# Kernel tuning notes

Measured on AMD Instinct MI355X. Metric: run time of the kernel, lower is better.

## Reference

```python
import jax, jax.numpy as jnp
import numpy as np

N_NODES = 50000
N_EDGES = 800000
D_IN = 256
D_OUT = 256


def setup_inputs() -> dict:
    key = jax.random.key(0)
    ks = jax.random.split(key, 8)
    x = jax.random.normal(ks[0], (N_NODES, D_IN), dtype=jnp.float32)
    edge_index = jax.random.randint(ks[1], (2, N_EDGES), 0, N_NODES, dtype=jnp.int64)
    W_src = jax.random.normal(ks[2], (D_IN, D_OUT), dtype=jnp.float32) * 0.05
    b_src = jax.random.normal(ks[3], (D_OUT,), dtype=jnp.float32) * 0.05
    W_dst = jax.random.normal(ks[4], (D_IN, D_OUT), dtype=jnp.float32) * 0.05
    b_dst = jax.random.normal(ks[5], (D_OUT,), dtype=jnp.float32) * 0.05
    W_self = jax.random.normal(ks[6], (D_IN, D_OUT), dtype=jnp.float32) * 0.05
    b_self = jax.random.normal(ks[7], (D_OUT,), dtype=jnp.float32) * 0.05
    return {"x": x, "edge_index": edge_index, "W_src": W_src, "b_src": b_src,
            "W_dst": W_dst, "b_dst": b_dst, "W_self": W_self, "b_self": b_self}


def reference(x, edge_index, W_src, b_src, W_dst, b_dst, W_self, b_self):
    # LEConv: messages = src_linear(x[row]) - dst_linear(x[col]);
    # scatter-add messages into destination nodes (col); add self_linear(x).
    # Linear commutes with row-gather, so project once on [N, d] then gather.
    row, col = edge_index[0], edge_index[1]
    src = x @ W_src + b_src            # [N, D_OUT]
    dst = x @ W_dst + b_dst            # [N, D_OUT]
    messages = src[row] - dst[col]     # [E, D_OUT]
    agg = jax.ops.segment_sum(messages, col, num_segments=x.shape[0])  # [N, D_OUT]
    return x @ W_self + b_self + agg
```

## Files before the change

### kernel.cpp

```cpp
#include <hip/hip_runtime.h>

#define D 256

typedef unsigned short ushort_t;
typedef unsigned int uint_t;
typedef __attribute__((ext_vector_type(8))) short short8;
typedef __attribute__((ext_vector_type(4))) float floatx4;

static __device__ __forceinline__ ushort_t f2bf(float f) {
    union { float f; uint_t u; } c; c.f = f;
    uint_t r = (c.u + 0x7FFFu + ((c.u >> 16) & 1u)) >> 16;
    return (ushort_t)r;
}
static __device__ __forceinline__ float bf2f(ushort_t b) {
    union { uint_t u; float f; } c; c.u = ((uint_t)b) << 16;
    return c.f;
}
static __device__ __forceinline__ uint_t scale2(uint_t v, float s) {
    ushort_t lo = (ushort_t)(v & 0xFFFFu), hi = (ushort_t)(v >> 16);
    return (uint_t)f2bf(bf2f(lo) * s) | ((uint_t)f2bf(bf2f(hi) * s) << 16);
}

static __device__ __forceinline__ void async16(const void* g, void* l) {
    __builtin_amdgcn_global_load_lds(
        (const __attribute__((address_space(1))) void*)g,
        (__attribute__((address_space(3))) void*)l, 16, 0, 0);
}

__global__ void prep_kernel(const int* __restrict__ col, int* __restrict__ deg,
                            int* __restrict__ rank,
                            const float* __restrict__ x, ushort_t* __restrict__ xh,
                            const float* __restrict__ Wself, const float* __restrict__ Wsrc,
                            const float* __restrict__ Wdst, ushort_t* __restrict__ BT,
                            int E, int total8, int degB, int cvtB) {
    int b = blockIdx.x;
    if (b < degB) {
        int e = b * 256 + threadIdx.x;
        if (e < E) rank[e] = atomicAdd(&deg[col[e]], 1);
    } else if (b < degB + cvtB) {
        int i = (b - degB) * 256 + threadIdx.x;
        if (i >= total8) return;
        float4 a = ((const float4*)x)[i * 2];
        float4 bb = ((const float4*)x)[i * 2 + 1];
        uint4 o;
        o.x = f2bf(a.x) | ((uint_t)f2bf(a.y) << 16);
        o.y = f2bf(a.z) | ((uint_t)f2bf(a.w) << 16);
        o.z = f2bf(bb.x) | ((uint_t)f2bf(bb.y) << 16);
        o.w = f2bf(bb.z) | ((uint_t)f2bf(bb.w) << 16);
        ((uint4*)xh)[i] = o;
    } else {
        int id = (b - degB - cvtB) * 256 + threadIdx.x;
        if (id >= 256 * 768) return;
        int j = id / 768, k = id % 768;
        float v;
        if (k < 256)      v =  Wself[(size_t)k * 256 + j];
        else if (k < 512) v =  Wsrc [(size_t)(k - 256) * 256 + j];
        else              v = -Wdst [(size_t)(k - 512) * 256 + j];
        BT[id] = f2bf(v);
    }
}

__global__ __launch_bounds__(256) void scanA(const int* __restrict__ deg,
                                             int* __restrict__ off,
                                             int* __restrict__ partials, int n4) {
    __shared__ int wtot[4];
    const int tid = threadIdx.x, lane = tid & 63, wid = tid >> 6;
    int i4 = blockIdx.x * 256 + tid;
    int4 v = (i4 < n4) ? ((const int4*)deg)[i4] : make_int4(0, 0, 0, 0);
    int s = v.x + v.y + v.z + v.w;
    int incl = s;
    #pragma unroll
    for (int st = 1; st < 64; st <<= 1) {
        int t = __shfl_up(incl, st, 64);
        if (lane >= st) incl += t;
    }
    if (lane == 63) wtot[wid] = incl;
    __syncthreads();
    int wbase = 0;
    #pragma unroll
    for (int w = 0; w < 4; ++w) if (w < wid) wbase += wtot[w];
    int excl = incl - s + wbase;
    if (i4 < n4) {
        int4 o;
        o.x = excl; o.y = o.x + v.x; o.z = o.y + v.y; o.w = o.z + v.z;
        ((int4*)off)[i4] = o;
    }
    if (tid == 0) partials[blockIdx.x] = wtot[0] + wtot[1] + wtot[2] + wtot[3];
}

__global__ __launch_bounds__(256) void scanC(int* __restrict__ off,
                                             const int* __restrict__ partials, int n4,
                                             const ushort_t* __restrict__ xh,
                                             const int* __restrict__ deg,
                                             ushort_t* __restrict__ Zh,
                                             int nblk, int totalChunks) {
    const int tid = threadIdx.x;
    int b = blockIdx.x;
    if (b < nblk) {
        __shared__ int base_s;
        if (tid < 64) {
            int v = (tid < b) ? partials[tid] : 0;
            #pragma unroll
            for (int st = 32; st; st >>= 1) v += __shfl_down(v, st, 64);
            if (tid == 0) base_s = v;
        }
        __syncthreads();
        int base = base_s;
        int i4 = b * 256 + tid;
        if (i4 < n4) {
            int4 o = ((int4*)off)[i4];
            o.x += base; o.y += base; o.z += base; o.w += base;
            ((int4*)off)[i4] = o;
        }
    } else {
        int c = (b - nblk) * 256 + tid;
        if (c >= totalChunks) return;
        int node = c >> 5;
        float s = (float)deg[node];
        uint4 v = ((const uint4*)xh)[c];
        uint4 o;
        o.x = scale2(v.x, s); o.y = scale2(v.y, s);
        o.z = scale2(v.z, s); o.w = scale2(v.w, s);
        ((uint4*)Zh)[c] = o;
    }
}

__global__ void fill_kernel(const int* __restrict__ row, const int* __restrict__ col,
                            const int* __restrict__ rank, const int* __restrict__ off,
                            int* __restrict__ bucket, int E) {
    int e = blockIdx.x * blockDim.x + threadIdx.x;
    if (e >= E) return;
    bucket[off[col[e]] + rank[e]] = row[e];
}

__global__ __launch_bounds__(256) void segsum_kernel(const ushort_t* __restrict__ xh,
                                                     const int* __restrict__ off,
                                                     const int* __restrict__ deg,
                                                     const int* __restrict__ bucket,
                                                     ushort_t* __restrict__ Gh, int N) {
    int node = blockIdx.x * 4 + (threadIdx.x >> 6);
    int lane = threadIdx.x & 63;
    if (node >= N) return;
    int start = off[node];
    int cnt = deg[node];
    float a0 = 0.f, a1 = 0.f, a2 = 0.f, a3 = 0.f;
    int i = 0;
    for (; i + 4 <= cnt; i += 4) {
        int r0 = bucket[start + i];
        int r1 = bucket[start + i + 1];
        int r2 = bucket[start + i + 2];
        int r3 = bucket[start + i + 3];
        ushort4 v0 = ((const ushort4*)(xh + (size_t)r0 * D))[lane];
        ushort4 v1 = ((const ushort4*)(xh + (size_t)r1 * D))[lane];
        ushort4 v2 = ((const ushort4*)(xh + (size_t)r2 * D))[lane];
        ushort4 v3 = ((const ushort4*)(xh + (size_t)r3 * D))[lane];
        a0 += (bf2f(v0.x) + bf2f(v1.x)) + (bf2f(v2.x) + bf2f(v3.x));
        a1 += (bf2f(v0.y) + bf2f(v1.y)) + (bf2f(v2.y) + bf2f(v3.y));
        a2 += (bf2f(v0.z) + bf2f(v1.z)) + (bf2f(v2.z) + bf2f(v3.z));
        a3 += (bf2f(v0.w) + bf2f(v1.w)) + (bf2f(v2.w) + bf2f(v3.w));
    }
    for (; i < cnt; ++i) {
        int r0 = bucket[start + i];
        ushort4 v0 = ((const ushort4*)(xh + (size_t)r0 * D))[lane];
        a0 += bf2f(v0.x); a1 += bf2f(v0.y); a2 += bf2f(v0.z); a3 += bf2f(v0.w);
    }
    ushort4 o;
    o.x = f2bf(a0); o.y = f2bf(a1); o.z = f2bf(a2); o.w = f2bf(a3);
    ((ushort4*)(Gh + (size_t)node * D))[lane] = o;
}

__global__ __launch_bounds__(256, 2) void mfma_gemm(
    const ushort_t* __restrict__ xh, const ushort_t* __restrict__ Gh,
    const ushort_t* __restrict__ Zh, const ushort_t* __restrict__ BT,
    const int* __restrict__ deg,
    const float* __restrict__ bsrc, const float* __restrict__ bdst,
    const float* __restrict__ bself, float* __restrict__ out, int N)
{
    __shared__ ushort_t As[2][8][64][8];
    __shared__ ushort_t Bs[2][16][64][8];

    const int tid = threadIdx.x;
    const int lane = tid & 63, wave = tid >> 6;
    const int quad = lane >> 4, l15 = lane & 15;
    const int mhalf = wave >> 1, nhalf = wave & 1;
    const int mbase = blockIdx.x * 128;

    const int ga0 = wave * 2, ga1 = ga0 + 1;
    int ar0 = mbase + ga0 * 16 + l15; if (ar0 >= N) ar0 = N - 1;
    int ar1 = mbase + ga1 * 16 + l15; if (ar1 >= N) ar1 = N - 1;
    const size_t aoff0 = (size_t)ar0 * 256 + quad * 8;
    const size_t aoff1 = (size_t)ar1 * 256 + quad * 8;
    const ushort_t* bp0 = BT + (size_t)((wave * 4 + 0) * 16 + l15) * 768 + quad * 8;
    const ushort_t* bp1 = BT + (size_t)((wave * 4 + 1) * 16 + l15) * 768 + quad * 8;
    const ushort_t* bp2 = BT + (size_t)((wave * 4 + 2) * 16 + l15) * 768 + quad * 8;
    const ushort_t* bp3 = BT + (size_t)((wave * 4 + 3) * 16 + l15) * 768 + quad * 8;
    const ushort_t* Asrc_[3] = {xh, Gh, Zh};

    floatx4 acc[4][8] = {};

    async16(xh + aoff0, &As[0][ga0][0][0]);
    async16(xh + aoff1, &As[0][ga1][0][0]);
    async16(bp0, &Bs[0][wave * 4 + 0][0][0]);
    async16(bp1, &Bs[0][wave * 4 + 1][0][0]);
    async16(bp2, &Bs[0][wave * 4 + 2][0][0]);
    async16(bp3, &Bs[0][wave * 4 + 3][0][0]);

    for (int kt = 0; kt < 24; ++kt) {
        const int cur = kt & 1;
        __syncthreads();
        if (kt < 23) {
            const int nk = kt + 1, nb = cur ^ 1;
            const ushort_t* s = Asrc_[nk >> 3];
            const int ka = (nk & 7) * 32;
            const int kb = nk * 32;
            async16(s + aoff0 + ka, &As[nb][ga0][0][0]);
            async16(s + aoff1 + ka, &As[nb][ga1][0][0]);
            async16(bp0 + kb, &Bs[nb][wave * 4 + 0][0][0]);
            async16(bp1 + kb, &Bs[nb][wave * 4 + 1][0][0]);
            async16(bp2 + kb, &Bs[nb][wave * 4 + 2][0][0]);
            async16(bp3 + kb, &Bs[nb][wave * 4 + 3][0][0]);
        }
        short8 af[4];
        #pragma unroll
        for (int im = 0; im < 4; ++im)
            af[im] = *(const short8*)(&As[cur][mhalf * 4 + im][lane][0]);
        #pragma unroll
        for (int h = 0; h < 2; ++h) {
            short8 bfr[4];
            #pragma unroll
            for (int in = 0; in < 4; ++in)
                bfr[in] = *(const short8*)(&Bs[cur][nhalf * 8 + h * 4 + in][lane][0]);
            #pragma unroll
            for (int im = 0; im < 4; ++im)
                #pragma unroll
                for (int in = 0; in < 4; ++in)
                    acc[im][h * 4 + in] = __builtin_amdgcn_mfma_f32_16x16x32_bf16(
                        af[im], bfr[in], acc[im][h * 4 + in], 0, 0, 0);
        }
    }

    float degv[4][4];
    #pragma unroll
    for (int im = 0; im < 4; ++im)
        #pragma unroll
        for (int r = 0; r < 4; ++r) {
            int gm = mbase + mhalf * 64 + im * 16 + quad * 4 + r;
            degv[im][r] = (gm < N) ? (float)deg[gm] : 0.f;
        }

    #pragma unroll
    for (int in = 0; in < 8; ++in) {
        int gn = nhalf * 128 + in * 16 + l15;
        float bs = bself[gn];
        float db = bsrc[gn] - bdst[gn];
        #pragma unroll
        for (int im = 0; im < 4; ++im) {
            #pragma unroll
            for (int r = 0; r < 4; ++r) {
                int gm = mbase + mhalf * 64 + im * 16 + quad * 4 + r;
                if (gm < N)
                    out[(size_t)gm * 256 + gn] = acc[im][in][r] + bs + degv[im][r] * db;
            }
        }
    }
}

extern "C" void kernel_launch(void* const* d_in, const int* in_sizes, int n_in,
                              void* d_out, int out_size, void* d_ws, size_t ws_size,
                              hipStream_t stream) {
    const float* x     = (const float*)d_in[0];
    const int*   eidx  = (const int*)d_in[1];
    const float* Wsrc  = (const float*)d_in[2];
    const float* bsrc  = (const float*)d_in[3];
    const float* Wdst  = (const float*)d_in[4];
    const float* bdst  = (const float*)d_in[5];
    const float* Wself = (const float*)d_in[6];
    const float* bself = (const float*)d_in[7];
    float* out = (float*)d_out;

    const int N = in_sizes[0] / D;
    const int E = in_sizes[1] / 2;
    const int* row = eidx;
    const int* col = eidx + E;

    char* p = (char*)d_ws;
    ushort_t* xh  = (ushort_t*)p;        p += (size_t)N * D * sizeof(ushort_t);
    ushort_t* Gh  = (ushort_t*)p;        int* rank = (int*)p;
                                         p += (size_t)N * D * sizeof(ushort_t);
    ushort_t* Zh  = (ushort_t*)p;        p += (size_t)N * D * sizeof(ushort_t);
    ushort_t* BT  = (ushort_t*)p;        p += (size_t)768 * 256 * sizeof(ushort_t);
    int* deg      = (int*)p;             p += (size_t)N * sizeof(int);
    int* off      = (int*)p;             p += (size_t)N * sizeof(int);
    int* partials = (int*)p;             p += 64 * sizeof(int);
    int* bucket   = (int*)p;

    hipMemsetAsync(deg, 0, (size_t)N * sizeof(int), stream);

    const int total8 = N * D / 8;
    const int degB = (E + 255) / 256;
    const int cvtB = (total8 + 255) / 256;
    const int btB  = (256 * 768 + 255) / 256;
    prep_kernel<<<degB + cvtB + btB, 256, 0, stream>>>(col, deg, rank, x, xh,
                                                       Wself, Wsrc, Wdst, BT,
                                                       E, total8, degB, cvtB);
    const int n4 = N / 4;
    const int nblk = (n4 + 255) / 256;
    scanA<<<nblk, 256, 0, stream>>>(deg, off, partials, n4);
    scanC<<<nblk + cvtB, 256, 0, stream>>>(off, partials, n4, xh, deg, Zh, nblk, total8);
    fill_kernel<<<(E + 255) / 256, 256, 0, stream>>>(row, col, rank, off, bucket, E);
    segsum_kernel<<<(N + 3) / 4, 256, 0, stream>>>(xh, off, deg, bucket, Gh, N);

    mfma_gemm<<<dim3((N + 127) / 128), 256, 0, stream>>>(
        xh, Gh, Zh, BT, deg, bsrc, bdst, bself, out, N);
}
```

Baseline: 285.7 us.

## Widen segsum loads to 16B per lane and drop LDS staging in GEMM

The segment-sum kernel now gives each node 32 lanes that each load 8 bf16 values (uint4), so a block covers 8 nodes and issues fewer, wider gathers. The GEMM no longer stages tiles through LDS with async global-to-LDS copies and barriers. Each wave reads its A and B fragments straight from global memory, working on a 64-row by 256-column tile with 3 blocks per CU. It also treats xh, Gh and Zh as one contiguous buffer. This removes LDS traffic and synchronisation, at the cost of redundant A loads across waves and less coalesced global reads that rely on cache hits.

```diff
diff --git a/kernel.cpp b/kernel.cpp
--- a/kernel.cpp
+++ b/kernel.cpp
@@ -20,11 +20,12 @@
     ushort_t lo = (ushort_t)(v & 0xFFFFu), hi = (ushort_t)(v >> 16);
     return (uint_t)f2bf(bf2f(lo) * s) | ((uint_t)f2bf(bf2f(hi) * s) << 16);
 }
-
-static __device__ __forceinline__ void async16(const void* g, void* l) {
-    __builtin_amdgcn_global_load_lds(
-        (const __attribute__((address_space(1))) void*)g,
-        (__attribute__((address_space(3))) void*)l, 16, 0, 0);
+static __device__ __forceinline__ void acc2(float& a, float& b, uint_t v) {
+    a += bf2f((ushort_t)(v & 0xFFFFu));
+    b += bf2f((ushort_t)(v >> 16));
+}
+static __device__ __forceinline__ uint_t pack2(float a, float b) {
+    return (uint_t)f2bf(a) | ((uint_t)f2bf(b) << 16);
 }
 
 __global__ void prep_kernel(const int* __restrict__ col, int* __restrict__ deg,
@@ -138,104 +139,82 @@
                                                      const int* __restrict__ deg,
                                                      const int* __restrict__ bucket,
                                                      ushort_t* __restrict__ Gh, int N) {
-    int node = blockIdx.x * 4 + (threadIdx.x >> 6);
-    int lane = threadIdx.x & 63;
+    int node = blockIdx.x * 8 + (threadIdx.x >> 5);
+    int lane31 = threadIdx.x & 31;
     if (node >= N) return;
     int start = off[node];
     int cnt = deg[node];
-    float a0 = 0.f, a1 = 0.f, a2 = 0.f, a3 = 0.f;
+    float a0 = 0.f, a1 = 0.f, a2 = 0.f, a3 = 0.f,
+          a4 = 0.f, a5 = 0.f, a6 = 0.f, a7 = 0.f;
     int i = 0;
     for (; i + 4 <= cnt; i += 4) {
         int r0 = bucket[start + i];
         int r1 = bucket[start + i + 1];
         int r2 = bucket[start + i + 2];
         int r3 = bucket[start + i + 3];
-        ushort4 v0 = ((const ushort4*)(xh + (size_t)r0 * D))[lane];
-        ushort4 v1 = ((const ushort4*)(xh + (size_t)r1 * D))[lane];
-        ushort4 v2 = ((const ushort4*)(xh + (size_t)r2 * D))[lane];
-        ushort4 v3 = ((const ushort4*)(xh + (size_t)r3 * D))[lane];
-        a0 += (bf2f(v0.x) + bf2f(v1.x)) + (bf2f(v2.x) + bf2f(v3.x));
-        a1 += (bf2f(v0.y) + bf2f(v1.y)) + (bf2f(v2.y) + bf2f(v3.y));
-        a2 += (bf2f(v0.z) + bf2f(v1.z)) + (bf2f(v2.z) + bf2f(v3.z));
-        a3 += (bf2f(v0.w) + bf2f(v1.w)) + (bf2f(v2.w) + bf2f(v3.w));
+        uint4 v0 = ((const uint4*)(xh + (size_t)r0 * D))[lane31];
+        uint4 v1 = ((const uint4*)(xh + (size_t)r1 * D))[lane31];
+        uint4 v2 = ((const uint4*)(xh + (size_t)r2 * D))[lane31];
+        uint4 v3 = ((const uint4*)(xh + (size_t)r3 * D))[lane31];
+        acc2(a0, a1, v0.x); acc2(a2, a3, v0.y); acc2(a4, a5, v0.z); acc2(a6, a7, v0.w);
+        acc2(a0, a1, v1.x); acc2(a2, a3, v1.y); acc2(a4, a5, v1.z); acc2(a6, a7, v1.w);
+        acc2(a0, a1, v2.x); acc2(a2, a3, v2.y); acc2(a4, a5, v2.z); acc2(a6, a7, v2.w);
+        acc2(a0, a1, v3.x); acc2(a2, a3, v3.y); acc2(a4, a5, v3.z); acc2(a6, a7, v3.w);
     }
     for (; i < cnt; ++i) {
         int r0 = bucket[start + i];
-        ushort4 v0 = ((const ushort4*)(xh + (size_t)r0 * D))[lane];
-        a0 += bf2f(v0.x); a1 += bf2f(v0.y); a2 += bf2f(v0.z); a3 += bf2f(v0.w);
-    }
-    ushort4 o;
-    o.x = f2bf(a0); o.y = f2bf(a1); o.z = f2bf(a2); o.w = f2bf(a3);
-    ((ushort4*)(Gh + (size_t)node * D))[lane] = o;
-}
-
-__global__ __launch_bounds__(256, 2) void mfma_gemm(
-    const ushort_t* __restrict__ xh, const ushort_t* __restrict__ Gh,
-    const ushort_t* __restrict__ Zh, const ushort_t* __restrict__ BT,
+        uint4 v0 = ((const uint4*)(xh + (size_t)r0 * D))[lane31];
+        acc2(a0, a1, v0.x); acc2(a2, a3, v0.y); acc2(a4, a5, v0.z); acc2(a6, a7, v0.w);
+    }
+    uint4 o;
+    o.x = pack2(a0, a1); o.y = pack2(a2, a3); o.z = pack2(a4, a5); o.w = pack2(a6, a7);
+    ((uint4*)(Gh + (size_t)node * D))[lane31] = o;
+}
+
+__global__ __launch_bounds__(256, 3) void mfma_gemm(
+    const ushort_t* __restrict__ A, const ushort_t* __restrict__ BT,
     const int* __restrict__ deg,
     const float* __restrict__ bsrc, const float* __restrict__ bdst,
     const float* __restrict__ bself, float* __restrict__ out, int N)
 {
-    __shared__ ushort_t As[2][8][64][8];
-    __shared__ ushort_t Bs[2][16][64][8];
-
     const int tid = threadIdx.x;
     const int lane = tid & 63, wave = tid >> 6;
     const int quad = lane >> 4, l15 = lane & 15;
-    const int mhalf = wave >> 1, nhalf = wave & 1;
-    const int mbase = blockIdx.x * 128;
-
-    const int ga0 = wave * 2, ga1 = ga0 + 1;
-    int ar0 = mbase + ga0 * 16 + l15; if (ar0 >= N) ar0 = N - 1;
-    int ar1 = mbase + ga1 * 16 + l15; if (ar1 >= N) ar1 = N - 1;
-    const size_t aoff0 = (size_t)ar0 * 256 + quad * 8;
-    const size_t aoff1 = (size_t)ar1 * 256 + quad * 8;
-    const ushort_t* bp0 = BT + (size_t)((wave * 4 + 0) * 16 + l15) * 768 + quad * 8;
-    const ushort_t* bp1 = BT + (size_t)((wave * 4 + 1) * 16 + l15) * 768 + quad * 8;
-    const ushort_t* bp2 = BT + (size_t)((wave * 4 + 2) * 16 + l15) * 768 + quad * 8;
-    const ushort_t* bp3 = BT + (size_t)((wave * 4 + 3) * 16 + l15) * 768 + quad * 8;
-    const ushort_t* Asrc_[3] = {xh, Gh, Zh};
-
-    floatx4 acc[4][8] = {};
-
-    async16(xh + aoff0, &As[0][ga0][0][0]);
-    async16(xh + aoff1, &As[0][ga1][0][0]);
-    async16(bp0, &Bs[0][wave * 4 + 0][0][0]);
-    async16(bp1, &Bs[0][wave * 4 + 1][0][0]);
-    async16(bp2, &Bs[0][wave * 4 + 2][0][0]);
-    async16(bp3, &Bs[0][wave * 4 + 3][0][0]);
-
-    for (int kt = 0; kt < 24; ++kt) {
-        const int cur = kt & 1;
-        __syncthreads();
-        if (kt < 23) {
-            const int nk = kt + 1, nb = cur ^ 1;
-            const ushort_t* s = Asrc_[nk >> 3];
-            const int ka = (nk & 7) * 32;
-            const int kb = nk * 32;
-            async16(s + aoff0 + ka, &As[nb][ga0][0][0]);
-            async16(s + aoff1 + ka, &As[nb][ga1][0][0]);
-            async16(bp0 + kb, &Bs[nb][wave * 4 + 0][0][0]);
-            async16(bp1 + kb, &Bs[nb][wave * 4 + 1][0][0]);
-            async16(bp2 + kb, &Bs[nb][wave * 4 + 2][0][0]);
-            async16(bp3 + kb, &Bs[nb][wave * 4 + 3][0][0]);
-        }
-        short8 af[4];
+    const int mbase = blockIdx.x * 64;
+
+    size_t arow[4];
+    #pragma unroll
+    for (int g = 0; g < 4; ++g) {
+        int r = mbase + g * 16 + l15;
+        if (r >= N) r = N - 1;
+        arow[g] = (size_t)r * 256 + quad * 8;
+    }
+    const ushort_t* bbase[4];
+    #pragma unroll
+    for (int g = 0; g < 4; ++g)
+        bbase[g] = BT + (size_t)((wave * 4 + g) * 16 + l15) * 768 + quad * 8;
+
+    floatx4 acc[4][4] = {};
+
+    #pragma unroll
+    for (int src = 0; src < 3; ++src) {
+        const ushort_t* Ab = A + (size_t)src * N * 256;
+        const int kb0 = src * 256;
         #pragma unroll
-        for (int im = 0; im < 4; ++im)
-            af[im] = *(const short8*)(&As[cur][mhalf * 4 + im][lane][0]);
-        #pragma unroll
-        for (int h = 0; h < 2; ++h) {
-            short8 bfr[4];
-            #pragma unroll
-            for (int in = 0; in < 4; ++in)
-                bfr[in] = *(const short8*)(&Bs[cur][nhalf * 8 + h * 4 + in][lane][0]);
+        for (int kk = 0; kk < 8; ++kk) {
+            short8 af[4], bfr[4];
+            #pragma unroll
+            for (int g = 0; g < 4; ++g)
+                af[g] = *(const short8*)(Ab + arow[g] + kk * 32);
+            #pragma unroll
+            for (int g = 0; g < 4; ++g)
+                bfr[g] = *(const short8*)(bbase[g] + kb0 + kk * 32);
             #pragma unroll
             for (int im = 0; im < 4; ++im)
                 #pragma unroll
                 for (int in = 0; in < 4; ++in)
-                    acc[im][h * 4 + in] = __builtin_amdgcn_mfma_f32_16x16x32_bf16(
-                        af[im], bfr[in], acc[im][h * 4 + in], 0, 0, 0);
+                    acc[im][in] = __builtin_amdgcn_mfma_f32_16x16x32_bf16(
+                        af[im], bfr[in], acc[im][in], 0, 0, 0);
         }
     }
 
@@ -244,20 +223,20 @@
     for (int im = 0; im < 4; ++im)
         #pragma unroll
         for (int r = 0; r < 4; ++r) {
-            int gm = mbase + mhalf * 64 + im * 16 + quad * 4 + r;
+            int gm = mbase + im * 16 + quad * 4 + r;
             degv[im][r] = (gm < N) ? (float)deg[gm] : 0.f;
         }
 
     #pragma unroll
-    for (int in = 0; in < 8; ++in) {
-        int gn = nhalf * 128 + in * 16 + l15;
+    for (int in = 0; in < 4; ++in) {
+        int gn = wave * 64 + in * 16 + l15;
         float bs = bself[gn];
         float db = bsrc[gn] - bdst[gn];
         #pragma unroll
         for (int im = 0; im < 4; ++im) {
             #pragma unroll
             for (int r = 0; r < 4; ++r) {
-                int gm = mbase + mhalf * 64 + im * 16 + quad * 4 + r;
+                int gm = mbase + im * 16 + quad * 4 + r;
                 if (gm < N)
                     out[(size_t)gm * 256 + gn] = acc[im][in][r] + bs + degv[im][r] * db;
             }
@@ -308,8 +287,8 @@
     scanA<<<nblk, 256, 0, stream>>>(deg, off, partials, n4);
     scanC<<<nblk + cvtB, 256, 0, stream>>>(off, partials, n4, xh, deg, Zh, nblk, total8);
     fill_kernel<<<(E + 255) / 256, 256, 0, stream>>>(row, col, rank, off, bucket, E);
-    segsum_kernel<<<(N + 3) / 4, 256, 0, stream>>>(xh, off, deg, bucket, Gh, N);
-
-    mfma_gemm<<<dim3((N + 127) / 128), 256, 0, stream>>>(
-        xh, Gh, Zh, BT, deg, bsrc, bdst, bself, out, N);
-}
+    segsum_kernel<<<(N + 7) / 8, 256, 0, stream>>>(xh, off, deg, bucket, Gh, N);
+
+    mfma_gemm<<<dim3((N + 63) / 64), 256, 0, stream>>>(
+        xh, BT, deg, bsrc, bdst, bself, out, N);
+}
```

After: 332.2 us. 16.3% more time.
